# Kernel optimization log

Measured on AMD Instinct MI355X. Metric: run time of the kernel, lower is better.

The kernel has to match this reference:

```python
import jax, jax.numpy as jnp
import numpy as np

EPS = 1e-5
K = 3          # deform conv kernel size
N = K * K      # 9 sampling points per output pixel


def conv2d(x, w, b=None):
    # x [B,C,H,W], w [O,I,kh,kw], stride 1, SAME padding (== torch padding=k//2)
    y = jax.lax.conv_general_dilated(x, w, (1, 1), 'SAME',
                                     dimension_numbers=('NCHW', 'OIHW', 'NCHW'))
    if b is not None:
        y = y + b[None, :, None, None]
    return y


def bilinear_sample(img, y, x):
    # img [B,C,H,W]; y,x [B,N,H,W] float sampling coordinates; zero padding outside.
    B, C, H, W = img.shape
    y0 = jnp.floor(y); x0 = jnp.floor(x)
    wy1 = y - y0; wy0 = 1.0 - wy1
    wx1 = x - x0; wx0 = 1.0 - wx1
    img_flat = img.reshape(B, C, H * W)

    def gather(yy, xx):
        valid = (yy >= 0) & (yy <= H - 1) & (xx >= 0) & (xx <= W - 1)
        yc = jnp.clip(yy, 0, H - 1).astype(jnp.int32)
        xc = jnp.clip(xx, 0, W - 1).astype(jnp.int32)
        idx = (yc * W + xc).reshape(B, -1)                      # [B, N*H*W]
        v = jax.vmap(lambda im, ix: im[:, ix])(img_flat, idx)   # [B, C, N*H*W]
        v = v.reshape(B, C, N, H, W)
        return v * valid[:, None].astype(img.dtype)

    v00 = gather(y0,     x0)
    v01 = gather(y0,     x0 + 1)
    v10 = gather(y0 + 1, x0)
    v11 = gather(y0 + 1, x0 + 1)
    wy0 = wy0[:, None]; wy1 = wy1[:, None]
    wx0 = wx0[:, None]; wx1 = wx1[:, None]
    return wy0 * (wx0 * v00 + wx1 * v01) + wy1 * (wx0 * v10 + wx1 * v11)


def deform_conv(x, w_off, b_off, w):
    # DeformConv2d(k=3, pad=1, stride=1, bias=False): offsets predicted by a 3x3 conv,
    # per-pixel bilinear sampling at p0 + pn + offset, then 3x3 weighted sum.
    B, C, H, W = x.shape
    off = conv2d(x, w_off, b_off)               # [B, 2N, H, W]
    dy, dx = off[:, :N], off[:, N:]
    ky, kx = jnp.meshgrid(jnp.arange(K) - 1, jnp.arange(K) - 1, indexing='ij')
    ky = ky.reshape(N).astype(x.dtype)
    kx = kx.reshape(N).astype(x.dtype)
    ii = jnp.arange(H, dtype=x.dtype)[None, None, :, None]
    jj = jnp.arange(W, dtype=x.dtype)[None, None, None, :]
    ysamp = ii + ky[None, :, None, None] + dy   # [B,N,H,W]
    xsamp = jj + kx[None, :, None, None] + dx
    s = bilinear_sample(x, ysamp, xsamp)        # [B,C,N,H,W]
    Cout = w.shape[0]
    return jnp.einsum('bcnhw,ocn->bohw', s, w.reshape(Cout, C, N))


def batchnorm_relu(x, gamma, beta):
    # train-mode BatchNorm2d (batch statistics, biased variance) + ReLU
    m = x.mean(axis=(0, 2, 3), keepdims=True)
    v = x.var(axis=(0, 2, 3), keepdims=True)
    xn = (x - m) * jax.lax.rsqrt(v + EPS)
    return jax.nn.relu(xn * gamma[None, :, None, None] + beta[None, :, None, None])


def maxpool2(x):
    return jax.lax.reduce_window(x, -jnp.inf, jax.lax.max,
                                 (1, 1, 2, 2), (1, 1, 2, 2), 'VALID')


def setup_inputs() -> dict:
    key = jax.random.key(0)
    ks = jax.random.split(key, 16)
    B, Cin, Cout, H, W = 4, 32, 64, 256, 256
    Hp, Wp = H // 2, W // 2
    f = jax.random.normal
    inp = {
        'x':  f(ks[0], (B, Cin, H, W), jnp.float32),
        'h0': f(ks[1], (B, Cout, Hp, Wp), jnp.float32),
        'c0': f(ks[2], (B, Cout, Hp, Wp), jnp.float32),
        # deform conv 1: Cin -> Cout
        'w_off1': f(ks[3], (2 * N, Cin, K, K), jnp.float32) * 0.01,
        'b_off1': jnp.zeros((2 * N,), jnp.float32),
        'w1': f(ks[4], (Cout, Cin, K, K), jnp.float32) * 0.05,
        'g1': jnp.ones((Cout,), jnp.float32),
        'be1': jnp.zeros((Cout,), jnp.float32),
        # deform conv 2: Cout -> Cout
        'w_off2': f(ks[5], (2 * N, Cout, K, K), jnp.float32) * 0.01,
        'b_off2': jnp.zeros((2 * N,), jnp.float32),
        'w2': f(ks[6], (Cout, Cout, K, K), jnp.float32) * 0.05,
        'g2': jnp.ones((Cout,), jnp.float32),
        'be2': jnp.zeros((Cout,), jnp.float32),
        # ConvLSTM gates: conv(cat(x, h)) -> 4*hidden channels
        'w_gates': f(ks[7], (4 * Cout, 2 * Cout, K, K), jnp.float32) * 0.05,
        'b_gates': jnp.zeros((4 * Cout,), jnp.float32),
    }
    return inp


def reference(x, h0, c0, w_off1, b_off1, w1, g1, be1,
              w_off2, b_off2, w2, g2, be2, w_gates, b_gates):
    # maxpool_conv = MaxPool2d(2) -> DoubleDConv (deform conv + BN + ReLU, twice)
    x = maxpool2(x)
    x = batchnorm_relu(deform_conv(x, w_off1, b_off1, w1), g1, be1)
    x = batchnorm_relu(deform_conv(x, w_off2, b_off2, w2), g2, be2)
    # ConvLSTM cell
    gates = conv2d(jnp.concatenate([x, h0], axis=1), w_gates, b_gates)
    i, f, o, g = jnp.split(gates, 4, axis=1)
    c = jax.nn.sigmoid(f) * c0 + jax.nn.sigmoid(i) * jnp.tanh(g)
    h = jax.nn.sigmoid(o) * jnp.tanh(c)
    # module returns (x, state) with x == hidden, state == (hidden, cell)
    return h, c
```

## Files before the change

### kernel.cpp

```cpp
#include <hip/hip_runtime.h>
#include <hip/hip_fp16.h>
#include <math.h>

#define P 128
#define NP (P*P)
#define BATCH 4

typedef __attribute__((ext_vector_type(8))) short bf16x8;
typedef __attribute__((ext_vector_type(4))) short s16x4;
typedef __attribute__((ext_vector_type(8))) _Float16 h16x8;
typedef __attribute__((ext_vector_type(4))) float f32x4;

__device__ __forceinline__ float sigmoidf_(float x){ return 1.f/(1.f+__expf(-x)); }
__device__ __forceinline__ float tanhf_(float x){
  float ax = fabsf(x);
  float e = __expf(2.f*ax);
  float t = 1.f - 2.f/(e + 1.f);
  return copysignf(t, x);
}
__device__ __forceinline__ short f2bf(float f){
  unsigned u = __builtin_bit_cast(unsigned, f);
  u = (u + 0x7FFFu + ((u>>16)&1u)) >> 16;
  return (short)u;
}
__device__ __forceinline__ float bf2f(short s){
  unsigned u = ((unsigned)(unsigned short)s) << 16;
  return __builtin_bit_cast(float, u);
}
__device__ __forceinline__ short f2h(float f){
  return (short)__half_as_short(__float2half(f));
}

__global__ void prep_k(const float* __restrict__ x, short* __restrict__ xph,
                       const float* __restrict__ h0, short* __restrict__ hcl,
                       const float* __restrict__ wg, const float* __restrict__ w1,
                       const float* __restrict__ w2, const float* __restrict__ wo1,
                       const float* __restrict__ wo2,
                       short* __restrict__ wA, short* __restrict__ wd1T,
                       short* __restrict__ wd2T, short* __restrict__ woT1,
                       short* __restrict__ woT2){
  int bx = blockIdx.x;
  int tid = threadIdx.x;
  if (bx < 256){
    int idx = bx*256 + tid;
    int wp = idx & (P-1); int t = idx >> 7; int hp = t & (P-1); int b = t >> 7;
    const float* src = x + ((size_t)b*32*65536) + (size_t)(hp*2)*256 + wp*2;
    float m[32];
    #pragma unroll
    for (int c = 0; c < 32; c++){
      const float* s = src + (size_t)c*65536;
      float2 t0 = *(const float2*)s;
      float2 t1 = *(const float2*)(s + 256);
      m[c] = fmaxf(fmaxf(t0.x, t0.y), fmaxf(t1.x, t1.y));
    }
    union { __half2 h[16]; h16x8 v[4]; } o;
    #pragma unroll
    for (int j = 0; j < 16; j++) o.h[j] = __float22half2_rn(float2{m[2*j], m[2*j+1]});
    short* dst = xph + (size_t)idx*32;
    #pragma unroll
    for (int q = 0; q < 4; q++) *(h16x8*)(dst + q*8) = o.v[q];
    return;
  }
  if (bx < 1280){
    __shared__ float t[64][65];
    int blk = bx - 256;
    int b = blk >> 8;
    int p0 = (blk & 255)*64;
    int pl = tid & 63;
    int cq = tid >> 6;
    const float* src = h0 + (size_t)b*64*NP + p0 + pl;
    #pragma unroll
    for (int i = 0; i < 16; i++)
      t[cq*16+i][pl] = src[(size_t)(cq*16+i)*NP];
    __syncthreads();
    int p = tid >> 2, q = tid & 3;
    short* dst = hcl + ((size_t)(b*NP + p0 + p))*64 + q*16;
    union { short s[8]; bf16x8 v; } o0, o1;
    #pragma unroll
    for (int i = 0; i < 8; i++){ o0.s[i] = f2bf(t[q*16+i][p]); o1.s[i] = f2bf(t[q*16+8+i][p]); }
    *(bf16x8*)dst = o0.v;
    *(bf16x8*)(dst+8) = o1.v;
    return;
  }
  int idx = (bx - 1280)*256 + tid;
  if (idx < 294912){
    int s = idx & 7; int l = (idx>>3) & 63; int mb = (idx>>9) & 15;
    int cb = (idx>>13) & 3; int tap = idx >> 15;
    int ln = l & 15, kg = l >> 4;
    int r = mb*16 + ln; int ch = r >> 2, gate = r & 3;
    int cin = cb*32 + kg*8 + s;
    wA[idx] = f2bf(wg[((size_t)(gate*64 + ch)*128 + cin)*9 + tap]);
    return;
  }
  idx -= 294912;
  if (idx < 18432){
    int s = idx & 7; int l = (idx>>3) & 63; int mb = (idx>>9) & 3; int tap = idx >> 11;
    int ln = l & 15, kg = l >> 4;
    int o = mb*16 + ln; int cin = kg*8 + s;
    wd1T[idx] = f2h(w1[((size_t)(o*32 + cin))*9 + tap]);
    return;
  }
  idx -= 18432;
  if (idx < 36864){
    int s = idx & 7; int l = (idx>>3) & 63; int mb = (idx>>9) & 3;
    int cb = (idx>>11) & 1; int tap = idx >> 12;
    int ln = l & 15, kg = l >> 4;
    int o = mb*16 + ln; int cin = cb*32 + kg*8 + s;
    wd2T[idx] = f2h(w2[((size_t)(o*64 + cin))*9 + tap]);
    return;
  }
  idx -= 36864;
  if (idx < 9216){
    int s = idx & 7; int l = (idx>>3) & 63; int mb = (idx>>9) & 1; int tap = idx >> 10;
    int ln = l & 15, kg = l >> 4;
    int o = mb*16 + ln; int cin = kg*8 + s;
    woT1[idx] = (o < 18) ? f2h(wo1[((size_t)(o*32 + cin))*9 + tap]) : (short)0;
    return;
  }
  idx -= 9216;
  if (idx < 18432){
    int s = idx & 7; int l = (idx>>3) & 63; int mb = (idx>>9) & 1;
    int cb = (idx>>10) & 1; int tap = idx >> 11;
    int ln = l & 15, kg = l >> 4;
    int o = mb*16 + ln; int cin = cb*32 + kg*8 + s;
    woT2[idx] = (o < 18) ? f2h(wo2[((size_t)(o*64 + cin))*9 + tap]) : (short)0;
  }
}

template<int CIN, bool BNIN, int INFMT>
__global__ __launch_bounds__(256) void deform_fused_k(
    const void* __restrict__ incl, const float* __restrict__ bstats,
    const float* __restrict__ b_off,
    const short* __restrict__ woT, const short* __restrict__ wdT,
    short* __restrict__ outb, float* __restrict__ part){
  const int HS = 14, NHP = HS*HS;
  const int ROWB = CIN*2;
  const int CG = CIN/8, CGS = (CIN==64)?3:2;
  const int PM = (CIN==64)?7:3;
  const int NCB = CIN/32;
  __shared__ short xt[NHP*CIN];
  __shared__ float off_lds[64][20];
  __shared__ float red_s[4][64], red_q[4][64];
  int tid = threadIdx.x;
  int tile = blockIdx.x, b = blockIdx.y;
  int tx0 = (tile & 15)*8, ty0 = (tile >> 4)*8;
  for (int e = tid; e < NHP*CG; e += 256){
    int cg = e & (CG-1), p = e >> CGS;
    int hr = p/HS, wc = p - hr*HS;
    int gy = ty0 + hr - 3, gx = tx0 + wc - 3;
    union { short s[8]; __half2 h[4]; h16x8 v; } u;
    bool ok = ((unsigned)gy < P) && ((unsigned)gx < P);
    if (ok){
      if constexpr (INFMT == 2 && !BNIN){
        u.v = *(const h16x8*)((const short*)incl + ((size_t)b*NP + (size_t)gy*P + gx)*CIN + cg*8);
      } else {
        float v[8];
        if constexpr (INFMT == 1){
          const short* src = (const short*)incl + ((size_t)b*NP + (size_t)gy*P + gx)*CIN + cg*8;
          bf16x8 raw = *(const bf16x8*)src;
          #pragma unroll
          for (int j = 0; j < 8; j++) v[j] = bf2f(raw[j]);
        } else if constexpr (INFMT == 2){
          const short* src = (const short*)incl + ((size_t)b*NP + (size_t)gy*P + gx)*CIN + cg*8;
          h16x8 raw = *(const h16x8*)(const void*)src;
          #pragma unroll
          for (int j = 0; j < 8; j++) v[j] = (float)raw[j];
        } else {
          const float* src = (const float*)incl + ((size_t)b*NP + (size_t)gy*P + gx)*CIN + cg*8;
          float4 a = *(const float4*)src, bb = *(const float4*)(src+4);
          v[0]=a.x; v[1]=a.y; v[2]=a.z; v[3]=a.w;
          v[4]=bb.x; v[5]=bb.y; v[6]=bb.z; v[7]=bb.w;
        }
        if (BNIN){
          int c = cg*8;
          #pragma unroll
          for (int j = 0; j < 8; j++) v[j] = fmaxf(v[j]*bstats[c+j]+bstats[64+c+j], 0.f);
        }
        u.h[0] = __float22half2_rn(float2{v[0], v[1]});
        u.h[1] = __float22half2_rn(float2{v[2], v[3]});
        u.h[2] = __float22half2_rn(float2{v[4], v[5]});
        u.h[3] = __float22half2_rn(float2{v[6], v[7]});
      }
    } else {
      #pragma unroll
      for (int j = 0; j < 8; j++) u.s[j] = 0;
    }
    *(h16x8*)((char*)xt + p*ROWB + ((cg*16) ^ ((p & PM)<<4))) = u.v;
  }
  __syncthreads();

  int lane = tid & 63, wid = tid >> 6;
  int kg = lane >> 4, ln = lane & 15;
  int py = ty0 + wid*2 + (ln>>3), pxg = tx0 + (ln&7);
  int pl = wid*16 + ln;

  {
    f32x4 acc_o[2];
    acc_o[0] = (f32x4){0.f,0.f,0.f,0.f};
    acc_o[1] = (f32x4){0.f,0.f,0.f,0.f};
    #pragma unroll
    for (int tap = 0; tap < 9; tap++){
      int ky = tap/3, kx = tap - (tap/3)*3;
      int lr = wid*2 + (ln>>3) + ky + 2;
      int lc = (ln&7) + kx + 2;
      int p = lr*HS + lc;
      #pragma unroll
      for (int cb = 0; cb < NCB; cb++){
        h16x8 bfv = *(const h16x8*)((const char*)xt + p*ROWB + (((cb*64) + kg*16) ^ ((p & PM)<<4)));
        h16x8 af0 = *(const h16x8*)(const void*)(woT + ((size_t)((tap*NCB + cb)*2 + 0)*512 + lane*8));
        h16x8 af1 = *(const h16x8*)(const void*)(woT + ((size_t)((tap*NCB + cb)*2 + 1)*512 + lane*8));
        acc_o[0] = __builtin_amdgcn_mfma_f32_16x16x32_f16(af0, bfv, acc_o[0], 0, 0, 0);
        acc_o[1] = __builtin_amdgcn_mfma_f32_16x16x32_f16(af1, bfv, acc_o[1], 0, 0, 0);
      }
    }
    #pragma unroll
    for (int mf = 0; mf < 2; mf++){
      #pragma unroll
      for (int j = 0; j < 4; j++){
        int o = mf*16 + kg*4 + j;
        if (o < 18) off_lds[pl][o] = acc_o[mf][j] + b_off[o];
      }
    }
  }
  __syncthreads();

  f32x4 acc[4];
  #pragma unroll
  for (int mf = 0; mf < 4; mf++) acc[mf] = (f32x4){0.f,0.f,0.f,0.f};

  for (int tap = 0; tap < 9; tap++){
    float dy = off_lds[pl][tap], dx = off_lds[pl][9+tap];
    float ys = (float)(py + tap/3 - 1) + dy;
    float xs = (float)(pxg + tap%3 - 1) + dx;
    float y0f = floorf(ys), x0f = floorf(xs);
    float wy1 = ys - y0f, wx1 = xs - x0f;
    float wy0 = 1.f - wy1, wx0 = 1.f - wx1;
    int y0 = (int)y0f, x0 = (int)x0f;
    bool v0y = ((unsigned)y0 < P), v1y = ((unsigned)(y0+1) < P);
    bool v0x = ((unsigned)x0 < P), v1x = ((unsigned)(x0+1) < P);
    float w00 = (v0y && v0x) ? wy0*wx0 : 0.f;
    float w01 = (v0y && v1x) ? wy0*wx1 : 0.f;
    float w10 = (v1y && v0x) ? wy1*wx0 : 0.f;
    float w11 = (v1y && v1x) ? wy1*wx1 : 0.f;
    __half2 w00h = __float2half2_rn(w00);
    __half2 w01h = __float2half2_rn(w01);
    __half2 w10h = __float2half2_rn(w10);
    __half2 w11h = __float2half2_rn(w11);
    int ly0 = min(max(y0 - ty0 + 3, 0), HS-1);
    int ly1 = min(max(y0 + 1 - ty0 + 3, 0), HS-1);
    int lx0 = min(max(x0 - tx0 + 3, 0), HS-1);
    int lx1 = min(max(x0 + 1 - tx0 + 3, 0), HS-1);
    int p00 = ly0*HS + lx0, p01 = ly0*HS + lx1;
    int p10 = ly1*HS + lx0, p11 = ly1*HS + lx1;
    #pragma unroll
    for (int cb = 0; cb < NCB; cb++){
      int ko = (cb*32 + kg*8)*2;
      union { __half2 h[4]; h16x8 v; } c00, c01, c10, c11, bu;
      c00.v = *(const h16x8*)((const char*)xt + p00*ROWB + (ko ^ ((p00 & PM)<<4)));
      c01.v = *(const h16x8*)((const char*)xt + p01*ROWB + (ko ^ ((p01 & PM)<<4)));
      c10.v = *(const h16x8*)((const char*)xt + p10*ROWB + (ko ^ ((p10 & PM)<<4)));
      c11.v = *(const h16x8*)((const char*)xt + p11*ROWB + (ko ^ ((p11 & PM)<<4)));
      #pragma unroll
      for (int j = 0; j < 4; j++){
        bu.h[j] = __hfma2(c00.h[j], w00h,
                  __hfma2(c01.h[j], w01h,
                  __hfma2(c10.h[j], w10h,
                  __hmul2(c11.h[j], w11h))));
      }
      #pragma unroll
      for (int mf = 0; mf < 4; mf++){
        h16x8 af = *(const h16x8*)(const void*)(wdT + ((size_t)((tap*NCB + cb)*4 + mf)*512 + lane*8));
        acc[mf] = __builtin_amdgcn_mfma_f32_16x16x32_f16(af, bu.v, acc[mf], 0, 0, 0);
      }
    }
  }
  #pragma unroll
  for (int mf = 0; mf < 4; mf++){
    short* dst = outb + ((size_t)b*NP + (size_t)py*P + pxg)*64 + mf*16 + kg*4;
    s16x4 o;
    #pragma unroll
    for (int j = 0; j < 4; j++) o[j] = f2bf(acc[mf][j]);
    *(s16x4*)dst = o;
  }

  #pragma unroll
  for (int mf = 0; mf < 4; mf++){
    #pragma unroll
    for (int j = 0; j < 4; j++){
      float s = acc[mf][j], q = s*s;
      #pragma unroll
      for (int o = 1; o < 16; o <<= 1){
        s += __shfl_xor(s, o);
        q += __shfl_xor(q, o);
      }
      if (ln == 0){
        int ch = mf*16 + kg*4 + j;
        red_s[wid][ch] = s;
        red_q[wid][ch] = q;
      }
    }
  }
  __syncthreads();
  int blk = b*256 + tile;
  if (tid < 128){
    int ch = tid & 63;
    float v = (tid < 64)
      ? (red_s[0][ch]+red_s[1][ch]+red_s[2][ch]+red_s[3][ch])
      : (red_q[0][ch]+red_q[1][ch]+red_q[2][ch]+red_q[3][ch]);
    part[(size_t)tid*1024 + blk] = v;
  }
}

__global__ void bnfinal2_k(const float* __restrict__ part, const float* __restrict__ g,
                           const float* __restrict__ be, float* __restrict__ stats){
  int ch = blockIdx.x;
  int tid = threadIdx.x;
  float S = 0.f, Q = 0.f;
  for (int i = tid; i < 1024; i += 256){
    S += part[(size_t)ch*1024 + i];
    Q += part[(size_t)(64+ch)*1024 + i];
  }
  __shared__ float rs[256], rq[256];
  rs[tid] = S; rq[tid] = Q;
  __syncthreads();
  for (int o = 128; o > 0; o >>= 1){
    if (tid < o){ rs[tid] += rs[tid+o]; rq[tid] += rq[tid+o]; }
    __syncthreads();
  }
  if (tid == 0){
    const float inv = 1.f/(float)(BATCH*NP);
    float mean = rs[0]*inv;
    float var = rq[0]*inv - mean*mean;
    float scale = rsqrtf(var + 1e-5f)*g[ch];
    stats[ch] = scale;
    stats[64+ch] = be[ch] - mean*scale;
  }
}

__global__ __launch_bounds__(512, 4) void gates_mfma_k(
    const short* __restrict__ y2b, const float* __restrict__ stats,
    const short* __restrict__ hcl, const float* __restrict__ c0,
    const short* __restrict__ wA, const float* __restrict__ bg,
    float* __restrict__ outh, float* __restrict__ outc){
  extern __shared__ short lds[];
  short* bs = lds;
  short* abuf = lds + 180*128;
  int tid = threadIdx.x;
  int tile = blockIdx.x, b = blockIdx.y;
  int tx0 = (tile & 7)*16, ty0 = (tile >> 3)*8;
  int lane = tid & 63, wid = tid >> 6;

  for (int e = tid; e < 180*16; e += 512){
    int cg = e & 15, p = e >> 4;
    int hr = p/18, wc = p - hr*18;
    int gy = ty0 + hr - 1, gx = tx0 + wc - 1;
    union { short s[8]; bf16x8 v; } u;
    if (((unsigned)gy < P) && ((unsigned)gx < P)){
      if (cg < 8){
        const short* src = y2b + ((size_t)(b*NP) + (size_t)gy*P + gx)*64 + cg*8;
        bf16x8 raw = *(const bf16x8*)src;
        int c = cg*8;
        #pragma unroll
        for (int j = 0; j < 8; j++){
          float v = fmaxf(bf2f(raw[j])*stats[c+j] + stats[64+c+j], 0.f);
          u.s[j] = f2bf(v);
        }
      } else {
        u.v = *(const bf16x8*)(hcl + ((size_t)(b*NP) + (size_t)gy*P + gx)*64 + (cg-8)*8);
      }
    } else {
      #pragma unroll
      for (int j = 0; j < 8; j++) u.s[j] = 0;
    }
    *(bf16x8*)((char*)bs + p*256 + ((cg*16) ^ ((p&7)<<4))) = u.v;
  }

  auto stageA = [&](int c, int bi){
    const short* g = wA + (size_t)c*8192;
    short* l = abuf + bi*8192;
    #pragma unroll
    for (int i = 0; i < 2; i++){
      int unit = wid*2 + i;
      __builtin_amdgcn_global_load_lds(
          (const __attribute__((address_space(1))) unsigned int*)(g + (size_t)(unit*64 + lane)*8),
          (__attribute__((address_space(3))) unsigned int*)(l + (size_t)unit*512),
          16, 0, 0);
    }
  };

  stageA(0, 0);
  stageA(1, 1);
  __syncthreads();

  int kg = lane >> 4, ln = lane & 15;
  int ct = wid >> 1, nh = wid & 1;
  f32x4 acc[4][4];
  #pragma unroll
  for (int mf = 0; mf < 4; mf++)
    #pragma unroll
    for (int rr = 0; rr < 4; rr++) acc[mf][rr] = (f32x4){0.f,0.f,0.f,0.f};

  for (int c = 0; c < 36; c++){
    int cur = c & 1;
    int tap = c >> 2, cb = c & 3;
    int ky = tap/3, kx = tap - ky*3;
    const short* al = abuf + cur*8192;
    bf16x8 af[4], bf[4];
    #pragma unroll
    for (int mf = 0; mf < 4; mf++)
      af[mf] = *(const bf16x8*)(al + (size_t)(ct*4 + mf)*512 + lane*8);
    #pragma unroll
    for (int rr = 0; rr < 4; rr++){
      int p = (nh*4 + rr + ky)*18 + ln + kx;
      bf[rr] = *(const bf16x8*)((const char*)bs + p*256 + (((cb*64) + kg*16) ^ ((p&7)<<4)));
    }
    asm volatile("s_waitcnt lgkmcnt(0)" ::: "memory");
    __builtin_amdgcn_sched_barrier(0);
    __builtin_amdgcn_s_setprio(1);
    #pragma unroll
    for (int rr = 0; rr < 4; rr++)
      #pragma unroll
      for (int mf = 0; mf < 4; mf++)
        acc[mf][rr] = __builtin_amdgcn_mfma_f32_16x16x32_bf16(af[mf], bf[rr], acc[mf][rr], 0, 0, 0);
    __builtin_amdgcn_s_setprio(0);
    asm volatile("s_waitcnt vmcnt(0)" ::: "memory");
    __builtin_amdgcn_sched_barrier(0);
    __builtin_amdgcn_s_barrier();
    __builtin_amdgcn_sched_barrier(0);
    if (c + 2 < 36) stageA(c + 2, cur);
  }

  #pragma unroll
  for (int mf = 0; mf < 4; mf++){
    int ch = ct*16 + mf*4 + kg;
    float bi = bg[ch], bff = bg[64+ch], bo = bg[128+ch], bgv = bg[192+ch];
    #pragma unroll
    for (int rr = 0; rr < 4; rr++){
      int py = ty0 + nh*4 + rr, px = tx0 + ln;
      size_t pidx = ((size_t)(b*64 + ch))*NP + (size_t)py*P + px;
      f32x4 a = acc[mf][rr];
      float cv = sigmoidf_(a[1]+bff)*c0[pidx] + sigmoidf_(a[0]+bi)*tanhf_(a[3]+bgv);
      float hv = sigmoidf_(a[2]+bo)*tanhf_(cv);
      outh[pidx] = hv;
      outc[pidx] = cv;
    }
  }
}

extern "C" void kernel_launch(void* const* d_in, const int* in_sizes, int n_in,
                              void* d_out, int out_size, void* d_ws, size_t ws_size,
                              hipStream_t stream) {
  const float* x      = (const float*)d_in[0];
  const float* h0     = (const float*)d_in[1];
  const float* c0     = (const float*)d_in[2];
  const float* w_off1 = (const float*)d_in[3];
  const float* b_off1 = (const float*)d_in[4];
  const float* w1     = (const float*)d_in[5];
  const float* g1     = (const float*)d_in[6];
  const float* be1    = (const float*)d_in[7];
  const float* w_off2 = (const float*)d_in[8];
  const float* b_off2 = (const float*)d_in[9];
  const float* w2     = (const float*)d_in[10];
  const float* g2     = (const float*)d_in[11];
  const float* be2    = (const float*)d_in[12];
  const float* wg     = (const float*)d_in[13];
  const float* bg     = (const float*)d_in[14];

  float* ws     = (float*)d_ws;
  short* xph    = (short*)ws;
  short* hcl    = (short*)(ws + 1048576);
  short* y1b    = (short*)(ws + 3145728);
  short* y2b    = (short*)(ws + 5242880);
  float* part   = ws + 7340032;
  float* stats1 = ws + 7471104;
  float* stats2 = ws + 7471232;
  short* wA     = (short*)(ws + 7471360);
  short* wd1T   = wA + 294912;
  short* wd2T   = wd1T + 18432;
  short* woT1   = wd2T + 36864;
  short* woT2   = woT1 + 9216;

  (void)hipFuncSetAttribute((const void*)gates_mfma_k,
                            hipFuncAttributeMaxDynamicSharedMemorySize, 78848);

  prep_k<<<dim3(256 + 1024 + 1476), dim3(256), 0, stream>>>(
      x, xph, h0, hcl, wg, w1, w2, w_off1, w_off2, wA, wd1T, wd2T, woT1, woT2);

  deform_fused_k<32,false,2><<<dim3(256, BATCH), dim3(256), 0, stream>>>(
      xph, stats1, b_off1, woT1, wd1T, y1b, part);
  bnfinal2_k<<<dim3(64), dim3(256), 0, stream>>>(part, g1, be1, stats1);

  deform_fused_k<64,true,1><<<dim3(256, BATCH), dim3(256), 0, stream>>>(
      y1b, stats1, b_off2, woT2, wd2T, y2b, part);
  bnfinal2_k<<<dim3(64), dim3(256), 0, stream>>>(part, g2, be2, stats2);

  float* outh = (float*)d_out;
  float* outc = outh + (size_t)BATCH*64*NP;
  gates_mfma_k<<<dim3(128, BATCH), dim3(512), 78848, stream>>>(
      y2b, stats2, hcl, c0, wA, bg, outh, outc);
}
```

Measured before the change: 109.9 us.

## Enlarge deform conv tiles to 16x8 with two N-fragments per wave

The fused deform-conv kernel now processes a 16x8 output tile per block instead of 8x8. Each wave handles two 16-pixel rows (two N fragments), so the halo overhead per output pixel shrinks and the MFMA weight fragments loaded from global memory are reused across both fragments. Grid size and the BN partial-sum buffer halve to match, and the workspace offsets shift accordingly. The cost is more LDS per block (22x14 halo), more accumulator registers, and only 512 blocks per launch, which may reduce occupancy and parallelism.

```diff
diff --git a/kernel.cpp b/kernel.cpp
--- a/kernel.cpp
+++ b/kernel.cpp
@@ -133,20 +133,20 @@
     const float* __restrict__ b_off,
     const short* __restrict__ woT, const short* __restrict__ wdT,
     short* __restrict__ outb, float* __restrict__ part){
-  const int HS = 14, NHP = HS*HS;
+  const int HSX = 22, HSY = 14, NHP = HSX*HSY;
   const int ROWB = CIN*2;
   const int CG = CIN/8, CGS = (CIN==64)?3:2;
   const int PM = (CIN==64)?7:3;
   const int NCB = CIN/32;
   __shared__ short xt[NHP*CIN];
-  __shared__ float off_lds[64][20];
+  __shared__ float off_lds[128][20];
   __shared__ float red_s[4][64], red_q[4][64];
   int tid = threadIdx.x;
   int tile = blockIdx.x, b = blockIdx.y;
-  int tx0 = (tile & 15)*8, ty0 = (tile >> 4)*8;
+  int tx0 = (tile & 7)*16, ty0 = (tile >> 3)*8;
   for (int e = tid; e < NHP*CG; e += 256){
     int cg = e & (CG-1), p = e >> CGS;
-    int hr = p/HS, wc = p - hr*HS;
+    int hr = p/HSX, wc = p - hr*HSX;
     int gy = ty0 + hr - 3, gx = tx0 + wc - 3;
     union { short s[8]; __half2 h[4]; h16x8 v; } u;
     bool ok = ((unsigned)gy < P) && ((unsigned)gx < P);
@@ -191,103 +191,124 @@
 
   int lane = tid & 63, wid = tid >> 6;
   int kg = lane >> 4, ln = lane & 15;
-  int py = ty0 + wid*2 + (ln>>3), pxg = tx0 + (ln&7);
-  int pl = wid*16 + ln;
+  int pxg = tx0 + ln;
 
   {
-    f32x4 acc_o[2];
-    acc_o[0] = (f32x4){0.f,0.f,0.f,0.f};
-    acc_o[1] = (f32x4){0.f,0.f,0.f,0.f};
+    f32x4 acc_o[2][2];
+    #pragma unroll
+    for (int mf = 0; mf < 2; mf++)
+      #pragma unroll
+      for (int nf = 0; nf < 2; nf++) acc_o[mf][nf] = (f32x4){0.f,0.f,0.f,0.f};
     #pragma unroll
     for (int tap = 0; tap < 9; tap++){
       int ky = tap/3, kx = tap - (tap/3)*3;
-      int lr = wid*2 + (ln>>3) + ky + 2;
-      int lc = (ln&7) + kx + 2;
-      int p = lr*HS + lc;
-      #pragma unroll
-      for (int cb = 0; cb < NCB; cb++){
-        h16x8 bfv = *(const h16x8*)((const char*)xt + p*ROWB + (((cb*64) + kg*16) ^ ((p & PM)<<4)));
-        h16x8 af0 = *(const h16x8*)(const void*)(woT + ((size_t)((tap*NCB + cb)*2 + 0)*512 + lane*8));
-        h16x8 af1 = *(const h16x8*)(const void*)(woT + ((size_t)((tap*NCB + cb)*2 + 1)*512 + lane*8));
-        acc_o[0] = __builtin_amdgcn_mfma_f32_16x16x32_f16(af0, bfv, acc_o[0], 0, 0, 0);
-        acc_o[1] = __builtin_amdgcn_mfma_f32_16x16x32_f16(af1, bfv, acc_o[1], 0, 0, 0);
-      }
-    }
-    #pragma unroll
-    for (int mf = 0; mf < 2; mf++){
-      #pragma unroll
-      for (int j = 0; j < 4; j++){
-        int o = mf*16 + kg*4 + j;
-        if (o < 18) off_lds[pl][o] = acc_o[mf][j] + b_off[o];
+      #pragma unroll
+      for (int nf = 0; nf < 2; nf++){
+        int p = (wid*2 + nf + ky + 2)*HSX + (ln + kx + 2);
+        #pragma unroll
+        for (int cb = 0; cb < NCB; cb++){
+          h16x8 bfv = *(const h16x8*)((const char*)xt + p*ROWB + (((cb*64) + kg*16) ^ ((p & PM)<<4)));
+          h16x8 af0 = *(const h16x8*)(const void*)(woT + ((size_t)((tap*NCB + cb)*2 + 0)*512 + lane*8));
+          h16x8 af1 = *(const h16x8*)(const void*)(woT + ((size_t)((tap*NCB + cb)*2 + 1)*512 + lane*8));
+          acc_o[0][nf] = __builtin_amdgcn_mfma_f32_16x16x32_f16(af0, bfv, acc_o[0][nf], 0, 0, 0);
+          acc_o[1][nf] = __builtin_amdgcn_mfma_f32_16x16x32_f16(af1, bfv, acc_o[1][nf], 0, 0, 0);
+        }
+      }
+    }
+    #pragma unroll
+    for (int nf = 0; nf < 2; nf++){
+      int pl = wid*32 + nf*16 + ln;
+      #pragma unroll
+      for (int mf = 0; mf < 2; mf++){
+        #pragma unroll
+        for (int j = 0; j < 4; j++){
+          int o = mf*16 + kg*4 + j;
+          if (o < 18) off_lds[pl][o] = acc_o[mf][nf][j] + b_off[o];
+        }
       }
     }
   }
   __syncthreads();
 
-  f32x4 acc[4];
+  f32x4 acc[4][2];
   #pragma unroll
-  for (int mf = 0; mf < 4; mf++) acc[mf] = (f32x4){0.f,0.f,0.f,0.f};
+  for (int mf = 0; mf < 4; mf++)
+    #pragma unroll
+    for (int nf = 0; nf < 2; nf++) acc[mf][nf] = (f32x4){0.f,0.f,0.f,0.f};
 
   for (int tap = 0; tap < 9; tap++){
-    float dy = off_lds[pl][tap], dx = off_lds[pl][9+tap];
-    float ys = (float)(py + tap/3 - 1) + dy;
-    float xs = (float)(pxg + tap%3 - 1) + dx;
-    float y0f = floorf(ys), x0f = floorf(xs);
-    float wy1 = ys - y0f, wx1 = xs - x0f;
-    float wy0 = 1.f - wy1, wx0 = 1.f - wx1;
-    int y0 = (int)y0f, x0 = (int)x0f;
-    bool v0y = ((unsigned)y0 < P), v1y = ((unsigned)(y0+1) < P);
-    bool v0x = ((unsigned)x0 < P), v1x = ((unsigned)(x0+1) < P);
-    float w00 = (v0y && v0x) ? wy0*wx0 : 0.f;
-    float w01 = (v0y && v1x) ? wy0*wx1 : 0.f;
-    float w10 = (v1y && v0x) ? wy1*wx0 : 0.f;
-    float w11 = (v1y && v1x) ? wy1*wx1 : 0.f;
-    __half2 w00h = __float2half2_rn(w00);
-    __half2 w01h = __float2half2_rn(w01);
-    __half2 w10h = __float2half2_rn(w10);
-    __half2 w11h = __float2half2_rn(w11);
-    int ly0 = min(max(y0 - ty0 + 3, 0), HS-1);
-    int ly1 = min(max(y0 + 1 - ty0 + 3, 0), HS-1);
-    int lx0 = min(max(x0 - tx0 + 3, 0), HS-1);
-    int lx1 = min(max(x0 + 1 - tx0 + 3, 0), HS-1);
-    int p00 = ly0*HS + lx0, p01 = ly0*HS + lx1;
-    int p10 = ly1*HS + lx0, p11 = ly1*HS + lx1;
+    __half2 w00h[2], w01h[2], w10h[2], w11h[2];
+    int p00[2], p01[2], p10[2], p11[2];
+    #pragma unroll
+    for (int nf = 0; nf < 2; nf++){
+      int pl = wid*32 + nf*16 + ln;
+      int py = ty0 + wid*2 + nf;
+      float dy = off_lds[pl][tap], dx = off_lds[pl][9+tap];
+      float ys = (float)(py + tap/3 - 1) + dy;
+      float xs = (float)(pxg + tap%3 - 1) + dx;
+      float y0f = floorf(ys), x0f = floorf(xs);
+      float wy1 = ys - y0f, wx1 = xs - x0f;
+      float wy0 = 1.f - wy1, wx0 = 1.f - wx1;
+      int y0 = (int)y0f, x0 = (int)x0f;
+      bool v0y = ((unsigned)y0 < P), v1y = ((unsigned)(y0+1) < P);
+      bool v0x = ((unsigned)x0 < P), v1x = ((unsigned)(x0+1) < P);
+      w00h[nf] = __float2half2_rn((v0y && v0x) ? wy0*wx0 : 0.f);
+      w01h[nf] = __float2half2_rn((v0y && v1x) ? wy0*wx1 : 0.f);
+      w10h[nf] = __float2half2_rn((v1y && v0x) ? wy1*wx0 : 0.f);
+      w11h[nf] = __float2half2_rn((v1y && v1x) ? wy1*wx1 : 0.f);
+      int ly0 = min(max(y0 - ty0 + 3, 0), HSY-1);
+      int ly1 = min(max(y0 + 1 - ty0 + 3, 0), HSY-1);
+      int lx0 = min(max(x0 - tx0 + 3, 0), HSX-1);
+      int lx1 = min(max(x0 + 1 - tx0 + 3, 0), HSX-1);
+      p00[nf] = ly0*HSX + lx0; p01[nf] = ly0*HSX + lx1;
+      p10[nf] = ly1*HSX + lx0; p11[nf] = ly1*HSX + lx1;
+    }
     #pragma unroll
     for (int cb = 0; cb < NCB; cb++){
       int ko = (cb*32 + kg*8)*2;
-      union { __half2 h[4]; h16x8 v; } c00, c01, c10, c11, bu;
-      c00.v = *(const h16x8*)((const char*)xt + p00*ROWB + (ko ^ ((p00 & PM)<<4)));
-      c01.v = *(const h16x8*)((const char*)xt + p01*ROWB + (ko ^ ((p01 & PM)<<4)));
-      c10.v = *(const h16x8*)((const char*)xt + p10*ROWB + (ko ^ ((p10 & PM)<<4)));
-      c11.v = *(const h16x8*)((const char*)xt + p11*ROWB + (ko ^ ((p11 & PM)<<4)));
-      #pragma unroll
-      for (int j = 0; j < 4; j++){
-        bu.h[j] = __hfma2(c00.h[j], w00h,
-                  __hfma2(c01.h[j], w01h,
-                  __hfma2(c10.h[j], w10h,
-                  __hmul2(c11.h[j], w11h))));
-      }
-      #pragma unroll
-      for (int mf = 0; mf < 4; mf++){
-        h16x8 af = *(const h16x8*)(const void*)(wdT + ((size_t)((tap*NCB + cb)*4 + mf)*512 + lane*8));
-        acc[mf] = __builtin_amdgcn_mfma_f32_16x16x32_f16(af, bu.v, acc[mf], 0, 0, 0);
-      }
-    }
-  }
+      h16x8 af[4];
+      #pragma unroll
+      for (int mf = 0; mf < 4; mf++)
+        af[mf] = *(const h16x8*)(const void*)(wdT + ((size_t)((tap*NCB + cb)*4 + mf)*512 + lane*8));
+      #pragma unroll
+      for (int nf = 0; nf < 2; nf++){
+        union { __half2 h[4]; h16x8 v; } c00, c01, c10, c11, bu;
+        c00.v = *(const h16x8*)((const char*)xt + p00[nf]*ROWB + (ko ^ ((p00[nf] & PM)<<4)));
+        c01.v = *(const h16x8*)((const char*)xt + p01[nf]*ROWB + (ko ^ ((p01[nf] & PM)<<4)));
+        c10.v = *(const h16x8*)((const char*)xt + p10[nf]*ROWB + (ko ^ ((p10[nf] & PM)<<4)));
+        c11.v = *(const h16x8*)((const char*)xt + p11[nf]*ROWB + (ko ^ ((p11[nf] & PM)<<4)));
+        #pragma unroll
+        for (int j = 0; j < 4; j++){
+          bu.h[j] = __hfma2(c00.h[j], w00h[nf],
+                    __hfma2(c01.h[j], w01h[nf],
+                    __hfma2(c10.h[j], w10h[nf],
+                    __hmul2(c11.h[j], w11h[nf]))));
+        }
+        #pragma unroll
+        for (int mf = 0; mf < 4; mf++)
+          acc[mf][nf] = __builtin_amdgcn_mfma_f32_16x16x32_f16(af[mf], bu.v, acc[mf][nf], 0, 0, 0);
+      }
+    }
+  }
+  #pragma unroll
+  for (int nf = 0; nf < 2; nf++){
+    int py = ty0 + wid*2 + nf;
+    #pragma unroll
+    for (int mf = 0; mf < 4; mf++){
+      short* dst = outb + ((size_t)b*NP + (size_t)py*P + pxg)*64 + mf*16 + kg*4;
+      s16x4 o;
+      #pragma unroll
+      for (int j = 0; j < 4; j++) o[j] = f2bf(acc[mf][nf][j]);
+      *(s16x4*)dst = o;
+    }
+  }
+
   #pragma unroll
   for (int mf = 0; mf < 4; mf++){
-    short* dst = outb + ((size_t)b*NP + (size_t)py*P + pxg)*64 + mf*16 + kg*4;
-    s16x4 o;
-    #pragma unroll
-    for (int j = 0; j < 4; j++) o[j] = f2bf(acc[mf][j]);
-    *(s16x4*)dst = o;
-  }
-
-  #pragma unroll
-  for (int mf = 0; mf < 4; mf++){
     #pragma unroll
     for (int j = 0; j < 4; j++){
-      float s = acc[mf][j], q = s*s;
+      float a0 = acc[mf][0][j], a1 = acc[mf][1][j];
+      float s = a0 + a1, q = a0*a0 + a1*a1;
       #pragma unroll
       for (int o = 1; o < 16; o <<= 1){
         s += __shfl_xor(s, o);
@@ -301,13 +322,13 @@
     }
   }
   __syncthreads();
-  int blk = b*256 + tile;
+  int blk = b*128 + tile;
   if (tid < 128){
     int ch = tid & 63;
     float v = (tid < 64)
       ? (red_s[0][ch]+red_s[1][ch]+red_s[2][ch]+red_s[3][ch])
       : (red_q[0][ch]+red_q[1][ch]+red_q[2][ch]+red_q[3][ch]);
-    part[(size_t)tid*1024 + blk] = v;
+    part[(size_t)tid*512 + blk] = v;
   }
 }
 
@@ -316,9 +337,9 @@
   int ch = blockIdx.x;
   int tid = threadIdx.x;
   float S = 0.f, Q = 0.f;
-  for (int i = tid; i < 1024; i += 256){
-    S += part[(size_t)ch*1024 + i];
-    Q += part[(size_t)(64+ch)*1024 + i];
+  for (int i = tid; i < 512; i += 256){
+    S += part[(size_t)ch*512 + i];
+    Q += part[(size_t)(64+ch)*512 + i];
   }
   __shared__ float rs[256], rq[256];
   rs[tid] = S; rq[tid] = Q;
@@ -472,9 +493,9 @@
   short* y1b    = (short*)(ws + 3145728);
   short* y2b    = (short*)(ws + 5242880);
   float* part   = ws + 7340032;
-  float* stats1 = ws + 7471104;
-  float* stats2 = ws + 7471232;
-  short* wA     = (short*)(ws + 7471360);
+  float* stats1 = ws + 7405568;
+  float* stats2 = ws + 7405696;
+  short* wA     = (short*)(ws + 7405824);
   short* wd1T   = wA + 294912;
   short* wd2T   = wd1T + 18432;
   short* woT1   = wd2T + 36864;
@@ -486,11 +507,11 @@
   prep_k<<<dim3(256 + 1024 + 1476), dim3(256), 0, stream>>>(
       x, xph, h0, hcl, wg, w1, w2, w_off1, w_off2, wA, wd1T, wd2T, woT1, woT2);
 
-  deform_fused_k<32,false,2><<<dim3(256, BATCH), dim3(256), 0, stream>>>(
+  deform_fused_k<32,false,2><<<dim3(128, BATCH), dim3(256), 0, stream>>>(
       xph, stats1, b_off1, woT1, wd1T, y1b, part);
   bnfinal2_k<<<dim3(64), dim3(256), 0, stream>>>(part, g1, be1, stats1);
 
-  deform_fused_k<64,true,1><<<dim3(256, BATCH), dim3(256), 0, stream>>>(
+  deform_fused_k<64,true,1><<<dim3(128, BATCH), dim3(256), 0, stream>>>(
       y1b, stats1, b_off2, woT2, wd2T, y2b, part);
   bnfinal2_k<<<dim3(64), dim3(256), 0, stream>>>(part, g2, be2, stats2);
 
```

New measurement: 106.2 us (median of 2 runs). 1.04x faster.
